# Kernel optimization log

Measured on AMD Instinct MI355X. Metric: run time of the kernel, lower is better.

Reference implementation:

```python
import jax, jax.numpy as jnp
import numpy as np

B, N, D = 2, 2048, 1024
H = 16
HD = D // H  # head_dim for kq and v

def setup_inputs() -> dict:
    key = jax.random.key(0)
    ks = jax.random.split(key, 5)
    scale = 1.0 / np.sqrt(D)
    return {
        "x": jax.random.normal(ks[0], (B, N, D), dtype=jnp.float32),
        "Wq": jax.random.normal(ks[1], (D, D), dtype=jnp.float32) * scale,
        "Wk": jax.random.normal(ks[2], (D, D), dtype=jnp.float32) * scale,
        "Wv": jax.random.normal(ks[3], (D, D), dtype=jnp.float32) * scale,
        "Wo": jax.random.normal(ks[4], (D, D), dtype=jnp.float32) * scale,
        "bo": jnp.zeros((D,), dtype=jnp.float32),
    }

def reference(x, Wq, Wk, Wv, Wo, bo):
    b, n, _ = x.shape
    # projections; torch Linear computes x @ W.T
    q = (x @ Wq.T).reshape(b, n, H, HD).transpose(0, 2, 1, 3)  # [B,H,N,HD]
    k = (x @ Wk.T).reshape(b, n, H, HD).transpose(0, 2, 1, 3)
    v = (x @ Wv.T).reshape(b, n, H, HD).transpose(0, 2, 1, 3)
    scores = jnp.einsum('bhqd,bhkd->bhqk', q, k) / jnp.sqrt(jnp.asarray(HD, x.dtype))
    causal = jnp.tril(jnp.ones((n, n), dtype=bool))
    scores = jnp.where(causal, scores, jnp.asarray(-jnp.inf, scores.dtype))
    probs = jax.nn.softmax(scores, axis=-1)  # dropout p=0.0 (eval)
    out = jnp.einsum('bhqk,bhkd->bhqd', probs, v)  # [B,H,N,HD]
    out = out.transpose(0, 2, 1, 3).reshape(b, n, D)
    return out @ Wo.T + bo
```

## Files before the change

kernel.cpp:

```cpp
#include <hip/hip_runtime.h>
#include <hip/hip_bf16.h>


typedef __bf16 bf16;
typedef __bf16 bf16x4 __attribute__((ext_vector_type(4)));
typedef __bf16 bf16x8 __attribute__((ext_vector_type(8)));
typedef float f32x4 __attribute__((ext_vector_type(4)));
typedef unsigned int u32x4 __attribute__((ext_vector_type(4)));

__device__ __forceinline__ f32x4 mfma16(bf16x8 a, bf16x8 b, f32x4 c) {
    return __builtin_amdgcn_mfma_f32_16x16x32_bf16(a, b, c, 0, 0, 0);
}

__device__ __forceinline__ void gload16(const bf16* g, bf16* l) {
    __builtin_amdgcn_global_load_lds(
        (const __attribute__((address_space(1))) unsigned int*)g,
        (__attribute__((address_space(3))) unsigned int*)l, 16, 0, 0);
}

__device__ __forceinline__ unsigned pkbf16(float a, float b) {
    unsigned lo = (unsigned)__builtin_bit_cast(unsigned short, (bf16)a);
    unsigned hi = (unsigned)__builtin_bit_cast(unsigned short, (bf16)b);
    return lo | (hi << 16);
}

__global__ __launch_bounds__(256) void f2b_kernel(const float* __restrict__ in,
                                                  bf16* __restrict__ out, int n) {
    int i = (blockIdx.x * 256 + threadIdx.x) * 4;
    if (i >= n) return;
    float4 v = *(const float4*)&in[i];
    bf16x4 o;
    o.x = (bf16)v.x; o.y = (bf16)v.y; o.z = (bf16)v.z; o.w = (bf16)v.w;
    *(bf16x4*)&out[i] = o;
}

__global__ __launch_bounds__(256) void w2b_kernel(
    const float* __restrict__ w0, const float* __restrict__ w1,
    const float* __restrict__ w2, const float* __restrict__ w3,
    bf16* __restrict__ o0, bf16* __restrict__ o1,
    bf16* __restrict__ o2, bf16* __restrict__ o3) {
    int sel = blockIdx.x >> 10;
    const float* in = sel == 0 ? w0 : sel == 1 ? w1 : sel == 2 ? w2 : w3;
    bf16* out = sel == 0 ? o0 : sel == 1 ? o1 : sel == 2 ? o2 : o3;
    int i = ((blockIdx.x & 1023) * 256 + threadIdx.x) * 4;
    float4 v = *(const float4*)&in[i];
    bf16x4 o;
    o.x = (bf16)v.x; o.y = (bf16)v.y; o.z = (bf16)v.z; o.w = (bf16)v.w;
    *(bf16x4*)&out[i] = o;
}

template <int MODE>
__device__ __forceinline__ void gemm_body(const bf16* __restrict__ A,
                                          const bf16* __restrict__ B,
                                          bf16* __restrict__ Cb,
                                          float* __restrict__ Cf,
                                          const float* __restrict__ bias,
                                          float scale, int N, int K, int row0, int col0) {
    __shared__ alignas(16) bf16 sA[128 * 32];
    __shared__ alignas(16) bf16 sB[128 * 32];
    const int tid  = threadIdx.x;
    const int lane = tid & 63;
    const int wave = tid >> 6;
    const int wrow = (wave >> 1) * 64;
    const int wcol = (wave & 1) * 64;
    const int la = lane & 15, lb = lane >> 4;

    const f32x4 fzero = {0.f, 0.f, 0.f, 0.f};
    f32x4 acc[4][4];
#pragma unroll
    for (int m = 0; m < 4; ++m)
#pragma unroll
        for (int n = 0; n < 4; ++n) acc[m][n] = fzero;

    for (int k0 = 0; k0 < K; k0 += 32) {
#pragma unroll
        for (int i = 0; i < 2; ++i) {
            int idx = i * 256 + tid;
            int r = idx >> 2, s = idx & 3;
            gload16(&A[(size_t)(row0 + r) * K + k0 + s * 8], &sA[idx * 8]);
            gload16(&B[(size_t)(col0 + r) * K + k0 + s * 8], &sB[idx * 8]);
        }
        __syncthreads();
        bf16x8 af[4], bfv[4];
#pragma unroll
        for (int m = 0; m < 4; ++m)
            af[m] = *(const bf16x8*)&sA[(wrow + m * 16 + la) * 32 + lb * 8];
#pragma unroll
        for (int n = 0; n < 4; ++n)
            bfv[n] = *(const bf16x8*)&sB[(wcol + n * 16 + la) * 32 + lb * 8];
#pragma unroll
        for (int m = 0; m < 4; ++m)
#pragma unroll
            for (int n = 0; n < 4; ++n)
                acc[m][n] = mfma16(af[m], bfv[n], acc[m][n]);
        __syncthreads();
    }
#pragma unroll
    for (int m = 0; m < 4; ++m)
#pragma unroll
        for (int n = 0; n < 4; ++n) {
            int col = col0 + wcol + n * 16 + la;
            if (MODE == 2) {
                int hh = col >> 6, hd = col & 63;
                int hc = hd >> 4, lav = hd & 15;
                int sp = row0 + wrow + m * 16 + lb * 4;
                int ktile = sp >> 6, k = sp & 63;
                int c = k >> 4, q = k & 15;
                size_t addr = (size_t)(ktile * 16 + hh) * 4096 +
                              (size_t)(((hc * 2 + (c >> 1)) * 16 + lav) * 32 +
                                       (q >> 2) * 8 + (c & 1) * 4);
                bf16x4 o4;
#pragma unroll
                for (int r = 0; r < 4; ++r) o4[r] = (bf16)acc[m][n][r];
                *(bf16x4*)&Cb[addr] = o4;
            } else if (MODE == 3) {
                int hh = col >> 6, hd = col & 63;
#pragma unroll
                for (int r = 0; r < 4; ++r) {
                    int row = row0 + wrow + m * 16 + lb * 4 + r;
                    int ktile = row >> 6, key = row & 63;
                    size_t addr = (size_t)(ktile * 16 + hh) * 4096 +
                                  (size_t)((((key >> 4) * 2 + (hd >> 5)) * 16 +
                                            (key & 15)) * 32 +
                                           ((hd >> 3) & 3) * 8 + (hd & 7));
                    Cb[addr] = (bf16)acc[m][n][r];
                }
            } else {
#pragma unroll
                for (int r = 0; r < 4; ++r) {
                    int row = row0 + wrow + m * 16 + lb * 4 + r;
                    if (MODE == 1)
                        Cf[(size_t)row * N + col] = acc[m][n][r] + bias[col];
                    else
                        Cb[(size_t)row * N + col] = (bf16)(acc[m][n][r] * scale);
                }
            }
        }
}

__global__ __launch_bounds__(256) void gemm_qkv_kernel(
    const bf16* __restrict__ xb, const bf16* __restrict__ wq,
    const bf16* __restrict__ wk, const bf16* __restrict__ wv,
    bf16* __restrict__ Q, bf16* __restrict__ Kf, bf16* __restrict__ Vf) {
    int z = blockIdx.z;
    if (z == 2) {
        gemm_body<2>(xb, wv, Vf, nullptr, nullptr, 1.f, 1024, 1024,
                     blockIdx.x * 128, blockIdx.y * 128);
    } else if (z == 1) {
        gemm_body<3>(xb, wk, Kf, nullptr, nullptr, 1.f, 1024, 1024,
                     blockIdx.x * 128, blockIdx.y * 128);
    } else {
        gemm_body<0>(xb, wq, Q, nullptr, nullptr, 0.1803368801111204f, 1024, 1024,
                     blockIdx.x * 128, blockIdx.y * 128);
    }
}

__global__ __launch_bounds__(256) void gemm_out_kernel(
    const bf16* __restrict__ att, const bf16* __restrict__ wo,
    float* __restrict__ out, const float* __restrict__ bias) {
    gemm_body<1>(att, wo, nullptr, out, bias, 1.f, 1024, 1024,
                 blockIdx.x * 128, blockIdx.y * 128);
}

struct KF { bf16x8 f[4][2]; };

__global__ __launch_bounds__(256, 2) void attn_kernel(
    const bf16* __restrict__ Q, const bf16* __restrict__ Kf,
    const bf16* __restrict__ Vf, bf16* __restrict__ O) {
    const int lane = threadIdx.x & 63;
    const int wave = threadIdx.x >> 6;
    const int bid = blockIdx.x;
    const int bh = (bid & 7) * 4 + ((bid >> 3) & 3);
    const int slot = bid >> 5;
    const int qt = slot < 8 ? slot : 23 - slot;
    const int h = bh & 15;
    const int b = bh >> 4;
    const int q0w = qt * 128 + wave * 32;
    const int rowbase = b * 2048;
    const int la = lane & 15, lb = lane >> 4;
    const f32x4 fzero = {0.f, 0.f, 0.f, 0.f};
    const float C = 14.426950408889634f;
    const int colbase = h * 64;
    const int lane_off = la * 32 + lb * 8;

    bf16x8 aq[2][2];
#pragma unroll
    for (int mf = 0; mf < 2; ++mf) {
        const bf16* qp = &Q[(size_t)(rowbase + q0w + mf * 16 + la) * 1024 + colbase];
#pragma unroll
        for (int kc = 0; kc < 2; ++kc) aq[mf][kc] = *(const bf16x8*)(qp + kc * 32 + lb * 8);
    }

    bf16x8 bones;
#pragma unroll
    for (int j = 0; j < 8; ++j) bones[j] = (bf16)1.0f;

    f32x4 o[2][4], lacc[2];
#pragma unroll
    for (int mf = 0; mf < 2; ++mf) {
        lacc[mf] = fzero;
#pragma unroll
        for (int hc = 0; hc < 4; ++hc) o[mf][hc] = fzero;
    }

    const int nt = (q0w + 95) >> 6;

    KF ka, kb;
    {
        const bf16* kp = &Kf[(size_t)((b * 32 + 0) * 16 + h) * 4096 + lane_off];
#pragma unroll
        for (int ck = 0; ck < 4; ++ck) {
            ka.f[ck][0] = *(const bf16x8*)(kp + (ck * 2 + 0) * 512);
            ka.f[ck][1] = *(const bf16x8*)(kp + (ck * 2 + 1) * 512);
        }
    }

    auto TILE = [&](int tile, KF& kc, KF& kn, int pref) {
        const int k0 = tile * 64;
        const bool domask = (tile == nt - 1);
        bf16x8 bv[4][2];
        {
            const bf16* vp = &Vf[(size_t)((b * 32 + tile) * 16 + h) * 4096 + lane_off];
#pragma unroll
            for (int hc = 0; hc < 4; ++hc) {
                bv[hc][0] = *(const bf16x8*)(vp + (hc * 2 + 0) * 512);
                bv[hc][1] = *(const bf16x8*)(vp + (hc * 2 + 1) * 512);
            }
        }
        {
            const bf16* kp = &Kf[(size_t)((b * 32 + pref) * 16 + h) * 4096 + lane_off];
#pragma unroll
            for (int ck = 0; ck < 4; ++ck) {
                kn.f[ck][0] = *(const bf16x8*)(kp + (ck * 2 + 0) * 512);
                kn.f[ck][1] = *(const bf16x8*)(kp + (ck * 2 + 1) * 512);
            }
        }
        f32x4 s[2][4];
#pragma unroll
        for (int mf = 0; mf < 2; ++mf)
#pragma unroll
            for (int ck = 0; ck < 4; ++ck) s[mf][ck] = fzero;
#pragma unroll
        for (int ck = 0; ck < 4; ++ck)
#pragma unroll
            for (int mf = 0; mf < 2; ++mf) {
                s[mf][ck] = mfma16(kc.f[ck][0], aq[mf][0], s[mf][ck]);
                s[mf][ck] = mfma16(kc.f[ck][1], aq[mf][1], s[mf][ck]);
            }
        if (domask) {
#pragma unroll
            for (int mf = 0; mf < 2; ++mf) {
                int qrow = q0w + mf * 16 + la;
#pragma unroll
                for (int ck = 0; ck < 4; ++ck)
#pragma unroll
                    for (int r = 0; r < 4; ++r) {
                        int key = k0 + ck * 16 + lb * 4 + r;
                        if (key > qrow) s[mf][ck][r] = -1e30f;
                    }
            }
        }
        bf16x8 pa[2][2];
#pragma unroll
        for (int mf = 0; mf < 2; ++mf) {
            unsigned pk[4][2];
#pragma unroll
            for (int ck = 0; ck < 4; ++ck) {
                float p0 = __builtin_amdgcn_exp2f(s[mf][ck][0] - C);
                float p1 = __builtin_amdgcn_exp2f(s[mf][ck][1] - C);
                float p2 = __builtin_amdgcn_exp2f(s[mf][ck][2] - C);
                float p3 = __builtin_amdgcn_exp2f(s[mf][ck][3] - C);
                pk[ck][0] = pkbf16(p0, p1);
                pk[ck][1] = pkbf16(p2, p3);
            }
#pragma unroll
            for (int kc2 = 0; kc2 < 2; ++kc2) {
                u32x4 w;
                w.x = pk[kc2 * 2][0];
                w.y = pk[kc2 * 2][1];
                w.z = pk[kc2 * 2 + 1][0];
                w.w = pk[kc2 * 2 + 1][1];
                pa[mf][kc2] = __builtin_bit_cast(bf16x8, w);
            }
        }
#pragma unroll
        for (int hc = 0; hc < 4; ++hc)
#pragma unroll
            for (int mf = 0; mf < 2; ++mf) {
                o[mf][hc] = mfma16(pa[mf][0], bv[hc][0], o[mf][hc]);
                o[mf][hc] = mfma16(pa[mf][1], bv[hc][1], o[mf][hc]);
            }
#pragma unroll
        for (int mf = 0; mf < 2; ++mf) {
            lacc[mf] = mfma16(pa[mf][0], bones, lacc[mf]);
            lacc[mf] = mfma16(pa[mf][1], bones, lacc[mf]);
        }
    };

    int t = 0;
    for (; t + 2 <= nt; t += 2) {
        TILE(t, ka, kb, t + 1);
        TILE(t + 1, kb, ka, (t + 2 < nt ? t + 2 : nt - 1));
    }
    if (t < nt) TILE(t, ka, kb, nt - 1);

#pragma unroll
    for (int mf = 0; mf < 2; ++mf)
#pragma unroll
        for (int hc = 0; hc < 4; ++hc)
#pragma unroll
            for (int r = 0; r < 4; ++r) {
                int qrow = q0w + mf * 16 + lb * 4 + r;
                O[(size_t)(rowbase + qrow) * 1024 + colbase + hc * 16 + la] =
                    (bf16)(o[mf][hc][r] / lacc[mf][r]);
            }
}

extern "C" void kernel_launch(void* const* d_in, const int* in_sizes, int n_in,
                              void* d_out, int out_size, void* d_ws, size_t ws_size,
                              hipStream_t stream) {
    const float* x  = (const float*)d_in[0];
    const float* Wq = (const float*)d_in[1];
    const float* Wk = (const float*)d_in[2];
    const float* Wv = (const float*)d_in[3];
    const float* Wo = (const float*)d_in[4];
    const float* bo = (const float*)d_in[5];
    float* out = (float*)d_out;

    char* ws = (char*)d_ws;
    const size_t MB = 1024 * 1024;
    bf16* xb  = (bf16*)(ws + (size_t)0);
    bf16* wqb = (bf16*)(ws + 8 * MB);
    bf16* wkb = (bf16*)(ws + 10 * MB);
    bf16* wvb = (bf16*)(ws + 12 * MB);
    bf16* wob = (bf16*)(ws + 14 * MB);
    bf16* Qb  = (bf16*)(ws + 16 * MB);
    bf16* Kf  = (bf16*)(ws + 24 * MB);
    bf16* Vf  = (bf16*)(ws + 40 * MB);
    bf16* Ab  = (bf16*)(ws + 56 * MB);

    f2b_kernel<<<4096, 256, 0, stream>>>(x, xb, 4096 * 1024);
    w2b_kernel<<<4096, 256, 0, stream>>>(Wq, Wk, Wv, Wo, wqb, wkb, wvb, wob);

    gemm_qkv_kernel<<<dim3(32, 8, 3), 256, 0, stream>>>(xb, wqb, wkb, wvb, Qb, Kf, Vf);
    attn_kernel<<<512, 256, 0, stream>>>(Qb, Kf, Vf, Ab);
    gemm_out_kernel<<<dim3(32, 8), 256, 0, stream>>>(Ab, wob, out, bo);
}
```

Before: 102.5 us.

## Split attention key range across two wave groups and merge via LDS

Doubles the attention block to 512 threads, and each query sub-tile's key tiles are split between two wave groups. Each group accumulates unnormalized output and row sums over its half, then the second group writes its partials to shared memory and the first combines them and normalizes. The aim is shorter per-wave serial loops and more waves in flight for the long causal rows. The cost is extra LDS traffic, a block-wide barrier, and higher register/occupancy pressure at 512 threads. The merge is correct without a running max, since the softmax uses a fixed scale.

```diff
diff --git a/kernel.cpp b/kernel.cpp
--- a/kernel.cpp
+++ b/kernel.cpp
@@ -164,18 +164,22 @@
 
 struct KF { bf16x8 f[4][2]; };
 
-__global__ __launch_bounds__(256, 2) void attn_kernel(
+__global__ __launch_bounds__(512, 2) void attn_kernel(
     const bf16* __restrict__ Q, const bf16* __restrict__ Kf,
     const bf16* __restrict__ Vf, bf16* __restrict__ O) {
+    __shared__ f32x4 oLds[4][2][4][64];
+    __shared__ f32x4 lLds[4][2][64];
     const int lane = threadIdx.x & 63;
     const int wave = threadIdx.x >> 6;
+    const int qsub = wave & 3;
+    const int ksplit = wave >> 2;
     const int bid = blockIdx.x;
     const int bh = (bid & 7) * 4 + ((bid >> 3) & 3);
     const int slot = bid >> 5;
     const int qt = slot < 8 ? slot : 23 - slot;
     const int h = bh & 15;
     const int b = bh >> 4;
-    const int q0w = qt * 128 + wave * 32;
+    const int q0w = qt * 128 + qsub * 32;
     const int rowbase = b * 2048;
     const int la = lane & 15, lb = lane >> 4;
     const f32x4 fzero = {0.f, 0.f, 0.f, 0.f};
@@ -204,10 +208,13 @@
     }
 
     const int nt = (q0w + 95) >> 6;
+    const int half = nt >> 1;
+    const int t0 = ksplit ? half : 0;
+    const int t1 = ksplit ? nt : half;
 
     KF ka, kb;
-    {
-        const bf16* kp = &Kf[(size_t)((b * 32 + 0) * 16 + h) * 4096 + lane_off];
+    if (t0 < t1) {
+        const bf16* kp = &Kf[(size_t)((b * 32 + t0) * 16 + h) * 4096 + lane_off];
 #pragma unroll
         for (int ck = 0; ck < 4; ++ck) {
             ka.f[ck][0] = *(const bf16x8*)(kp + (ck * 2 + 0) * 512);
@@ -297,23 +304,41 @@
         }
     };
 
-    int t = 0;
-    for (; t + 2 <= nt; t += 2) {
+    int t = t0;
+    for (; t + 2 <= t1; t += 2) {
         TILE(t, ka, kb, t + 1);
-        TILE(t + 1, kb, ka, (t + 2 < nt ? t + 2 : nt - 1));
-    }
-    if (t < nt) TILE(t, ka, kb, nt - 1);
-
-#pragma unroll
-    for (int mf = 0; mf < 2; ++mf)
-#pragma unroll
-        for (int hc = 0; hc < 4; ++hc)
-#pragma unroll
-            for (int r = 0; r < 4; ++r) {
-                int qrow = q0w + mf * 16 + lb * 4 + r;
-                O[(size_t)(rowbase + qrow) * 1024 + colbase + hc * 16 + la] =
-                    (bf16)(o[mf][hc][r] / lacc[mf][r]);
-            }
+        TILE(t + 1, kb, ka, (t + 2 < t1 ? t + 2 : t1 - 1));
+    }
+    if (t < t1) TILE(t, ka, kb, t1 - 1);
+
+    if (ksplit == 1) {
+#pragma unroll
+        for (int mf = 0; mf < 2; ++mf) {
+#pragma unroll
+            for (int hc = 0; hc < 4; ++hc) oLds[qsub][mf][hc][lane] = o[mf][hc];
+            lLds[qsub][mf][lane] = lacc[mf];
+        }
+    }
+    __syncthreads();
+    if (ksplit == 0) {
+#pragma unroll
+        for (int mf = 0; mf < 2; ++mf) {
+            f32x4 lu = lLds[qsub][mf][lane];
+            f32x4 lt;
+#pragma unroll
+            for (int r = 0; r < 4; ++r) lt[r] = 1.0f / (lacc[mf][r] + lu[r]);
+#pragma unroll
+            for (int hc = 0; hc < 4; ++hc) {
+                f32x4 ou = oLds[qsub][mf][hc][lane];
+#pragma unroll
+                for (int r = 0; r < 4; ++r) {
+                    int qrow = q0w + mf * 16 + lb * 4 + r;
+                    O[(size_t)(rowbase + qrow) * 1024 + colbase + hc * 16 + la] =
+                        (bf16)((o[mf][hc][r] + ou[r]) * lt[r]);
+                }
+            }
+        }
+    }
 }
 
 extern "C" void kernel_launch(void* const* d_in, const int* in_sizes, int n_in,
@@ -343,6 +368,6 @@
     w2b_kernel<<<4096, 256, 0, stream>>>(Wq, Wk, Wv, Wo, wqb, wkb, wvb, wob);
 
     gemm_qkv_kernel<<<dim3(32, 8, 3), 256, 0, stream>>>(xb, wqb, wkb, wvb, Qb, Kf, Vf);
-    attn_kernel<<<512, 256, 0, stream>>>(Qb, Kf, Vf, Ab);
+    attn_kernel<<<512, 512, 0, stream>>>(Qb, Kf, Vf, Ab);
     gemm_out_kernel<<<dim3(32, 8), 256, 0, stream>>>(Ab, wob, out, bo);
 }
```

Result: slower. 104.8 us (+2.3%).

## Double-buffer V tiles in registers alongside K and raise MFMA wave priority

Applied to the files above, without the earlier changes.

V fragments for the next key tile are now prefetched one tile ahead into ping-pong registers, as K already was, instead of being loaded at the start of the tile that uses them. Tile pointers advance incrementally from a fixed base instead of being recomputed per tile. s_setprio is raised around the MFMA blocks so matrix work gets issue priority over other waves, and bf16 packing goes through a vector bitcast. The intent is to hide V load latency behind the previous tile's compute, at the cost of more VGPRs, which could reduce occupancy at the two-blocks-per-CU launch bound.

```diff
diff --git a/kernel.cpp b/kernel.cpp
--- a/kernel.cpp
+++ b/kernel.cpp
@@ -3,6 +3,7 @@
 
 
 typedef __bf16 bf16;
+typedef __bf16 bf16x2 __attribute__((ext_vector_type(2)));
 typedef __bf16 bf16x4 __attribute__((ext_vector_type(4)));
 typedef __bf16 bf16x8 __attribute__((ext_vector_type(8)));
 typedef float f32x4 __attribute__((ext_vector_type(4)));
@@ -18,10 +19,11 @@
         (__attribute__((address_space(3))) unsigned int*)l, 16, 0, 0);
 }
 
-__device__ __forceinline__ unsigned pkbf16(float a, float b) {
-    unsigned lo = (unsigned)__builtin_bit_cast(unsigned short, (bf16)a);
-    unsigned hi = (unsigned)__builtin_bit_cast(unsigned short, (bf16)b);
-    return lo | (hi << 16);
+__device__ __forceinline__ unsigned pk2(float a, float b) {
+    bf16x2 v;
+    v[0] = (bf16)a;
+    v[1] = (bf16)b;
+    return __builtin_bit_cast(unsigned, v);
 }
 
 __global__ __launch_bounds__(256) void f2b_kernel(const float* __restrict__ in,
@@ -182,6 +184,7 @@
     const float C = 14.426950408889634f;
     const int colbase = h * 64;
     const int lane_off = la * 32 + lb * 8;
+    const int TSTRIDE = 16 * 4096;
 
     bf16x8 aq[2][2];
 #pragma unroll
@@ -205,41 +208,38 @@
 
     const int nt = (q0w + 95) >> 6;
 
-    KF ka, kb;
-    {
-        const bf16* kp = &Kf[(size_t)((b * 32 + 0) * 16 + h) * 4096 + lane_off];
+    const bf16* kbase = &Kf[(size_t)(b * 32 * 16 + h) * 4096 + lane_off + 2048];
+    const bf16* vbase = &Vf[(size_t)(b * 32 * 16 + h) * 4096 + lane_off + 2048];
+
+    KF ka, kb, va, vb;
+#pragma unroll
+    for (int ck = 0; ck < 4; ++ck) {
+        ka.f[ck][0] = *(const bf16x8*)(kbase + (ck * 2 + 0) * 512 - 2048);
+        ka.f[ck][1] = *(const bf16x8*)(kbase + (ck * 2 + 1) * 512 - 2048);
+        va.f[ck][0] = *(const bf16x8*)(vbase + (ck * 2 + 0) * 512 - 2048);
+        va.f[ck][1] = *(const bf16x8*)(vbase + (ck * 2 + 1) * 512 - 2048);
+    }
+    const bf16* kpf = kbase + (nt > 1 ? TSTRIDE : 0);
+    const bf16* vpf = vbase + (nt > 1 ? TSTRIDE : 0);
+
+    auto TILE = [&](int t, KF& kc, KF& kn, KF& vc, KF& vn) {
+        const bool domask = (t == nt - 1);
 #pragma unroll
         for (int ck = 0; ck < 4; ++ck) {
-            ka.f[ck][0] = *(const bf16x8*)(kp + (ck * 2 + 0) * 512);
-            ka.f[ck][1] = *(const bf16x8*)(kp + (ck * 2 + 1) * 512);
-        }
-    }
-
-    auto TILE = [&](int tile, KF& kc, KF& kn, int pref) {
-        const int k0 = tile * 64;
-        const bool domask = (tile == nt - 1);
-        bf16x8 bv[4][2];
-        {
-            const bf16* vp = &Vf[(size_t)((b * 32 + tile) * 16 + h) * 4096 + lane_off];
-#pragma unroll
-            for (int hc = 0; hc < 4; ++hc) {
-                bv[hc][0] = *(const bf16x8*)(vp + (hc * 2 + 0) * 512);
-                bv[hc][1] = *(const bf16x8*)(vp + (hc * 2 + 1) * 512);
-            }
-        }
-        {
-            const bf16* kp = &Kf[(size_t)((b * 32 + pref) * 16 + h) * 4096 + lane_off];
-#pragma unroll
-            for (int ck = 0; ck < 4; ++ck) {
-                kn.f[ck][0] = *(const bf16x8*)(kp + (ck * 2 + 0) * 512);
-                kn.f[ck][1] = *(const bf16x8*)(kp + (ck * 2 + 1) * 512);
-            }
-        }
+            kn.f[ck][0] = *(const bf16x8*)(kpf + (ck * 2 + 0) * 512 - 2048);
+            kn.f[ck][1] = *(const bf16x8*)(kpf + (ck * 2 + 1) * 512 - 2048);
+            vn.f[ck][0] = *(const bf16x8*)(vpf + (ck * 2 + 0) * 512 - 2048);
+            vn.f[ck][1] = *(const bf16x8*)(vpf + (ck * 2 + 1) * 512 - 2048);
+        }
+        int adv = (t + 2 < nt) ? TSTRIDE : 0;
+        kpf += adv;
+        vpf += adv;
         f32x4 s[2][4];
 #pragma unroll
         for (int mf = 0; mf < 2; ++mf)
 #pragma unroll
             for (int ck = 0; ck < 4; ++ck) s[mf][ck] = fzero;
+        __builtin_amdgcn_s_setprio(1);
 #pragma unroll
         for (int ck = 0; ck < 4; ++ck)
 #pragma unroll
@@ -247,7 +247,9 @@
                 s[mf][ck] = mfma16(kc.f[ck][0], aq[mf][0], s[mf][ck]);
                 s[mf][ck] = mfma16(kc.f[ck][1], aq[mf][1], s[mf][ck]);
             }
+        __builtin_amdgcn_s_setprio(0);
         if (domask) {
+            const int k0 = t * 64;
 #pragma unroll
             for (int mf = 0; mf < 2; ++mf) {
                 int qrow = q0w + mf * 16 + la;
@@ -270,8 +272,8 @@
                 float p1 = __builtin_amdgcn_exp2f(s[mf][ck][1] - C);
                 float p2 = __builtin_amdgcn_exp2f(s[mf][ck][2] - C);
                 float p3 = __builtin_amdgcn_exp2f(s[mf][ck][3] - C);
-                pk[ck][0] = pkbf16(p0, p1);
-                pk[ck][1] = pkbf16(p2, p3);
+                pk[ck][0] = pk2(p0, p1);
+                pk[ck][1] = pk2(p2, p3);
             }
 #pragma unroll
             for (int kc2 = 0; kc2 < 2; ++kc2) {
@@ -283,26 +285,28 @@
                 pa[mf][kc2] = __builtin_bit_cast(bf16x8, w);
             }
         }
+        __builtin_amdgcn_s_setprio(1);
 #pragma unroll
         for (int hc = 0; hc < 4; ++hc)
 #pragma unroll
             for (int mf = 0; mf < 2; ++mf) {
-                o[mf][hc] = mfma16(pa[mf][0], bv[hc][0], o[mf][hc]);
-                o[mf][hc] = mfma16(pa[mf][1], bv[hc][1], o[mf][hc]);
+                o[mf][hc] = mfma16(pa[mf][0], vc.f[hc][0], o[mf][hc]);
+                o[mf][hc] = mfma16(pa[mf][1], vc.f[hc][1], o[mf][hc]);
             }
 #pragma unroll
         for (int mf = 0; mf < 2; ++mf) {
             lacc[mf] = mfma16(pa[mf][0], bones, lacc[mf]);
             lacc[mf] = mfma16(pa[mf][1], bones, lacc[mf]);
         }
+        __builtin_amdgcn_s_setprio(0);
     };
 
     int t = 0;
     for (; t + 2 <= nt; t += 2) {
-        TILE(t, ka, kb, t + 1);
-        TILE(t + 1, kb, ka, (t + 2 < nt ? t + 2 : nt - 1));
-    }
-    if (t < nt) TILE(t, ka, kb, nt - 1);
+        TILE(t, ka, kb, va, vb);
+        TILE(t + 1, kb, ka, vb, va);
+    }
+    if (t < nt) TILE(t, ka, kb, va, vb);
 
 #pragma unroll
     for (int mf = 0; mf < 2; ++mf)
```

After: 102.6 us. About the same (+0.1%).
